# Optimization experiments

Measured on AMD Instinct MI355X. Metric: run time of the kernel, lower is better.

Reference implementation:

```python
import math
import jax, jax.numpy as jnp
import numpy as np

CNT_HEAD, D_IN, D_OUT, D_KEY, D_VALUE = 16, 1024, 1024, 64, 64
BATCH, SEQ = 4, 2048
IS_SCALED, IS_CAUSAL = True, True


def _xavier(key, shape, d1, d2):
    a = math.sqrt(6.0 / (d1 + d2))
    return jax.random.uniform(key, shape, jnp.float32, -a, a)


def setup_inputs() -> dict:
    key = jax.random.key(0)
    kx, kq, kk, kv, ko = jax.random.split(key, 5)
    x = jax.random.normal(kx, (BATCH, SEQ, D_IN), jnp.float32)
    mask = jnp.zeros((BATCH, SEQ), dtype=bool)  # padding mask, True = masked out
    W_q = _xavier(kq, (CNT_HEAD, D_IN, D_KEY), D_IN, CNT_HEAD * D_KEY)
    W_k = _xavier(kk, (CNT_HEAD, D_IN, D_KEY), D_IN, CNT_HEAD * D_KEY)
    W_v = _xavier(kv, (CNT_HEAD, D_IN, D_VALUE), D_IN, CNT_HEAD * D_VALUE)
    W_o = _xavier(ko, (CNT_HEAD, D_VALUE, D_OUT), CNT_HEAD * D_VALUE, D_OUT)
    return {"x": x, "mask": mask, "W_q": W_q, "W_k": W_k, "W_v": W_v, "W_o": W_o}


def reference(x, mask, W_q, W_k, W_v, W_o):
    seq_len = x.shape[-2]
    # per-head projections: (h, d_in, d) x (b, s, d_in) -> (b, h, s, d)
    Q = jnp.einsum('hjk,bsj->bhsk', W_q, x)
    K = jnp.einsum('hjk,bsj->bhsk', W_k, x)
    V = jnp.einsum('hjk,bsj->bhsk', W_v, x)
    # combined mask -> (b, 1, s, s), True = masked
    causal = jnp.triu(jnp.ones((seq_len, seq_len), dtype=bool), k=1)
    if IS_CAUSAL:
        m = mask[..., None, :] | causal  # (b, s, s)
    else:
        m = jnp.broadcast_to(mask[..., None, :], (mask.shape[0], seq_len, seq_len))
    m = m[..., None, :, :]  # (b, 1, s, s)
    scores = jnp.einsum('bhik,bhjk->bhij', Q, K)
    scores = jnp.where(m, -jnp.inf, scores)
    if IS_SCALED:
        scores = scores / math.sqrt(D_KEY)
    weights = jax.nn.softmax(scores, axis=-1)
    values = jnp.einsum('bhij,bhjd->bhid', weights, V)
    return jnp.einsum('hjk,bhlj->blk', W_o, values)
```

## Files before the change

kernel.cpp:

```cpp
#include <hip/hip_runtime.h>
#include <hip/hip_bf16.h>

typedef __attribute__((ext_vector_type(4))) float f32x4;
typedef __attribute__((ext_vector_type(8))) short s16x8;
typedef __attribute__((ext_vector_type(8))) unsigned short u16x8;
typedef __attribute__((ext_vector_type(4))) unsigned short u16x4;

#define BATCH 4
#define SEQ   2048
#define DIN   1024
#define NHEAD 16
#define HD3   3072
#define DOUT  1024

__device__ __forceinline__ unsigned short f2bf(float f) {
  __hip_bfloat16 h = __float2bfloat16(f);
  return __builtin_bit_cast(unsigned short, h);
}

#if __has_builtin(__builtin_amdgcn_exp2f)
__device__ __forceinline__ float fast_exp2(float x) { return __builtin_amdgcn_exp2f(x); }
#else
__device__ __forceinline__ float fast_exp2(float x) { return exp2f(x); }
#endif

typedef const __attribute__((address_space(1))) unsigned int* gas_t;
typedef __attribute__((address_space(3))) unsigned int* las_t;
__device__ __forceinline__ void gload16(const void* g, void* l) {
  __builtin_amdgcn_global_load_lds((gas_t)g, (las_t)l, 16, 0, 0);
}

__device__ __forceinline__ int swz128(int row, int bc) {
  return row * 128 + (((bc & ~15) ^ ((row & 7) << 4)) | (bc & 15));
}

__global__ __launch_bounds__(256) void k_cvt_x(const float* __restrict__ x,
                                               unsigned short* __restrict__ xb, int n4) {
  int i = blockIdx.x * 256 + threadIdx.x;
  int stride = gridDim.x * 256;
  for (; i < n4; i += stride) {
    float4 v = reinterpret_cast<const float4*>(x)[i];
    ushort4 o;
    o.x = f2bf(v.x); o.y = f2bf(v.y); o.z = f2bf(v.z); o.w = f2bf(v.w);
    reinterpret_cast<ushort4*>(xb)[i] = o;
  }
}

__global__ __launch_bounds__(256) void k_cvt_w(const float* __restrict__ W,
                                               unsigned short* __restrict__ dst) {
  __shared__ float t[64][65];
  int h = blockIdx.x, j0 = blockIdx.y * 64;
  int c = threadIdx.x & 63, r0 = threadIdx.x >> 6;
#pragma unroll
  for (int r = r0; r < 64; r += 4)
    t[r][c] = W[h * 65536 + (j0 + r) * 64 + c];
  __syncthreads();
#pragma unroll
  for (int k = r0; k < 64; k += 4)
    dst[(size_t)(h * 64 + k) * 1024 + j0 + c] = f2bf(t[c][k]);
}

__global__ __launch_bounds__(256) void k_cvt_wo(const float* __restrict__ W,
                                                unsigned short* __restrict__ dst) {
  __shared__ float t[64][65];
  int h = blockIdx.x, n0 = blockIdx.y * 64;
  int c = threadIdx.x & 63, r0 = threadIdx.x >> 6;
#pragma unroll
  for (int d = r0; d < 64; d += 4)
    t[d][c] = W[h * 65536 + d * 1024 + n0 + c];
  __syncthreads();
#pragma unroll
  for (int n = r0; n < 64; n += 4)
    dst[(size_t)(n0 + n) * 1024 + h * 64 + c] = f2bf(t[c][n]);
}

__global__ __launch_bounds__(256) void k_transpose_v(const unsigned short* __restrict__ QKV,
                                                     unsigned short* __restrict__ Vt) {
  __shared__ unsigned short t[64 * 80];
  int tid = threadIdx.x;
  int s0 = blockIdx.x * 64;
  int h = blockIdx.y, b = blockIdx.z;
  const unsigned short* src = QKV + (size_t)b * SEQ * HD3 + 2048 + (size_t)h * 64;
#pragma unroll
  for (int c = 0; c < 2; ++c) {
    int slot = tid + c * 256;
    int s = slot >> 3, g = slot & 7;
    u16x8 v = *reinterpret_cast<const u16x8*>(src + (size_t)(s0 + s) * HD3 + g * 8);
    *reinterpret_cast<u16x8*>(&t[s * 80 + (g ^ (s >> 3)) * 8]) = v;
  }
  __syncthreads();
  unsigned short* dst = Vt + (size_t)(b * NHEAD + h) * 64 * SEQ + s0;
#pragma unroll
  for (int c = 0; c < 2; ++c) {
    int slot = tid + c * 256;
    int d = slot >> 3, c8 = slot & 7;
    u16x8 v;
#pragma unroll
    for (int j = 0; j < 8; ++j) {
      int s = c8 * 8 + j;
      v[j] = t[s * 80 + (((d >> 3) ^ c8) * 8) + (d & 7)];
    }
    *reinterpret_cast<u16x8*>(dst + (size_t)d * SEQ + c8 * 8) = v;
  }
}

__device__ __forceinline__ void stout(float* p, float v) { *p = v; }
__device__ __forceinline__ void stout(unsigned short* p, float v) { *p = f2bf(v); }

template <typename OutT>
__global__ __launch_bounds__(256) void gemm_bt(const unsigned short* __restrict__ A,
                                               const unsigned short* __restrict__ Bt,
                                               OutT* __restrict__ C, int M, int N, int K) {
  __shared__ unsigned short As[3][128 * 32];
  __shared__ unsigned short Bs[3][128 * 32];
  int tid = threadIdx.x, w = tid >> 6, lane = tid & 63;
  int lr = lane & 15, lk = lane >> 4;
  int m0 = blockIdx.x * 128, n0 = blockIdx.y * 128;
  int wm = (w >> 1) * 64, wn = (w & 1) * 64;
  const f32x4 z = {0.f, 0.f, 0.f, 0.f};
  f32x4 acc[4][4];
#pragma unroll
  for (int m = 0; m < 4; ++m)
#pragma unroll
    for (int n = 0; n < 4; ++n) acc[m][n] = z;

  int r0 = w * 32 + (lane >> 2);
  int r1 = r0 + 16;
  int scol = (((lane & 3) ^ ((lane >> 2) & 3)) * 8);
  const unsigned short* pA0 = A + (size_t)(m0 + r0) * K + scol;
  const unsigned short* pA1 = A + (size_t)(m0 + r1) * K + scol;
  const unsigned short* pB0 = Bt + (size_t)(n0 + r0) * K + scol;
  const unsigned short* pB1 = Bt + (size_t)(n0 + r1) * K + scol;

#define GSTAGE(bi_, ko_)                                              \
  {                                                                   \
    gload16(pA0 + (ko_), (char*)As[bi_] + (w * 2 + 0) * 1024);        \
    gload16(pB0 + (ko_), (char*)Bs[bi_] + (w * 2 + 0) * 1024);        \
    gload16(pA1 + (ko_), (char*)As[bi_] + (w * 2 + 1) * 1024);        \
    gload16(pB1 + (ko_), (char*)Bs[bi_] + (w * 2 + 1) * 1024);        \
  }

  GSTAGE(0, 0)
  GSTAGE(1, 32)
  asm volatile("s_waitcnt vmcnt(4)" ::: "memory");
  __builtin_amdgcn_s_barrier();
  asm volatile("" ::: "memory");

  const int T = K >> 5;
  int bi = 0;
  int cka = lk ^ (lr & 3);
  for (int t = 0; t < T; ++t) {
    if (t + 2 < T) {
      int bs = bi + 2; if (bs >= 3) bs -= 3;
      GSTAGE(bs, (t + 2) * 32)
    }
    s16x8 af[4], bfr[4];
#pragma unroll
    for (int m = 0; m < 4; ++m)
      af[m] = *reinterpret_cast<const s16x8*>(&As[bi][(wm + m * 16 + lr) * 32 + cka * 8]);
#pragma unroll
    for (int n = 0; n < 4; ++n)
      bfr[n] = *reinterpret_cast<const s16x8*>(&Bs[bi][(wn + n * 16 + lr) * 32 + cka * 8]);
#pragma unroll
    for (int m = 0; m < 4; ++m)
#pragma unroll
      for (int n = 0; n < 4; ++n)
        acc[m][n] = __builtin_amdgcn_mfma_f32_16x16x32_bf16(af[m], bfr[n], acc[m][n], 0, 0, 0);
    asm volatile("s_waitcnt lgkmcnt(0)" ::: "memory");
    if (t + 2 < T)
      asm volatile("s_waitcnt vmcnt(4)" ::: "memory");
    else
      asm volatile("s_waitcnt vmcnt(0)" ::: "memory");
    __builtin_amdgcn_s_barrier();
    asm volatile("" ::: "memory");
    if (++bi >= 3) bi = 0;
  }
#undef GSTAGE

#pragma unroll
  for (int m = 0; m < 4; ++m)
#pragma unroll
    for (int n = 0; n < 4; ++n)
#pragma unroll
      for (int r = 0; r < 4; ++r) {
        int row = m0 + wm + m * 16 + lk * 4 + r;
        int col = n0 + wn + n * 16 + lr;
        stout(&C[(size_t)row * N + col], acc[m][n][r]);
      }
}

__global__ __launch_bounds__(256) void attn_kernel(const unsigned short* __restrict__ QKV,
                                                   const unsigned short* __restrict__ Vt,
                                                   unsigned short* __restrict__ Oa) {
  __shared__ unsigned short Ks[3][64 * 64];
  __shared__ unsigned short Vs[3][64 * 64];
  int tid = threadIdx.x, w = tid >> 6, lane = tid & 63;
  int lr = lane & 15, lk = lane >> 4;
  int bx = blockIdx.x;
  int bh = bx & 63;
  int qbi = 15 - (bx >> 6);
  int h = bh & 15, b = bh >> 4;
  int q0 = qbi * 128 + w * 32;
  const unsigned short* base = QKV + (size_t)b * SEQ * HD3;
  const unsigned short* vtb = Vt + (size_t)(b * NHEAD + h) * 64 * SEQ;
  const float cl = 0.1803368801111204f;
  const f32x4 z = {0.f, 0.f, 0.f, 0.f};

  s16x8 qf[2][2];
#pragma unroll
  for (int mf = 0; mf < 2; ++mf)
#pragma unroll
    for (int kfi = 0; kfi < 2; ++kfi)
      qf[mf][kfi] = *reinterpret_cast<const s16x8*>(
          base + (size_t)(q0 + mf * 16 + lr) * HD3 + h * 64 + kfi * 32 + lk * 8);

  f32x4 o[4][2], lacc[2];
#pragma unroll
  for (int nfd = 0; nfd < 4; ++nfd)
#pragma unroll
    for (int mf = 0; mf < 2; ++mf) o[nfd][mf] = z;
  lacc[0] = z; lacc[1] = z;
  float m_[2] = {-1e30f, -1e30f};
  s16x8 ones;
#pragma unroll
  for (int e = 0; e < 8; ++e) ones[e] = (short)0x3F80;

  const int nt = qbi * 2 + 2;
  int srow0 = w * 16 + (lane >> 3);
  int cb = ((lane & 7) * 16);
  const unsigned short* kSrc = base + 1024 + h * 64;

#define STAGE(kt_, bi_)                                                                   \
  {                                                                                       \
    int kb_ = (kt_) * 64;                                                                 \
    _Pragma("unroll") for (int c = 0; c < 2; ++c) {                                       \
      int rr = srow0 + c * 8;                                                             \
      int cbs = cb ^ ((rr & 7) << 4);                                                     \
      gload16((const char*)(kSrc + (size_t)(kb_ + rr) * HD3) + cbs,                       \
              (char*)&Ks[bi_][0] + (w * 2 + c) * 1024);                                   \
      gload16((const char*)(vtb + (size_t)rr * SEQ + kb_) + cbs,                          \
              (char*)&Vs[bi_][0] + (w * 2 + c) * 1024);                                   \
    }                                                                                     \
  }

  STAGE(0, 0)
  STAGE(1, 1)
  asm volatile("s_waitcnt vmcnt(4)" ::: "memory");
  __builtin_amdgcn_s_barrier();
  asm volatile("" ::: "memory");

  int bi = 0;
  for (int kt = 0; kt < nt; ++kt) {
    if (kt + 2 < nt) {
      int bs = bi + 2; if (bs >= 3) bs -= 3;
      STAGE(kt + 2, bs)
    }
    const char* KB = (const char*)&Ks[bi][0];
    const char* VB = (const char*)&Vs[bi][0];

    s16x8 kfr[4][2];
#pragma unroll
    for (int nf = 0; nf < 4; ++nf)
#pragma unroll
      for (int kfi = 0; kfi < 2; ++kfi)
        kfr[nf][kfi] =
            *reinterpret_cast<const s16x8*>(KB + swz128(nf * 16 + lr, kfi * 64 + lk * 16));

    f32x4 st[4][2];
#pragma unroll
    for (int nf = 0; nf < 4; ++nf)
#pragma unroll
      for (int mf = 0; mf < 2; ++mf)
        st[nf][mf] = __builtin_amdgcn_mfma_f32_16x16x32_bf16(kfr[nf][0], qf[mf][0], z, 0, 0, 0);
#pragma unroll
    for (int nf = 0; nf < 4; ++nf)
#pragma unroll
      for (int mf = 0; mf < 2; ++mf)
        st[nf][mf] =
            __builtin_amdgcn_mfma_f32_16x16x32_bf16(kfr[nf][1], qf[mf][1], st[nf][mf], 0, 0, 0);

    if (kt >= nt - 2) {
      int kb = kt * 64;
#pragma unroll
      for (int nf = 0; nf < 4; ++nf)
#pragma unroll
        for (int mf = 0; mf < 2; ++mf)
#pragma unroll
          for (int r = 0; r < 4; ++r)
            if (kb + nf * 16 + lk * 4 + r > q0 + mf * 16 + lr) st[nf][mf][r] = -1e30f;
    }

    s16x8 pf[2][2];
#pragma unroll
    for (int mf = 0; mf < 2; ++mf) {
      float pm = fmaxf(fmaxf(fmaxf(st[0][mf][0], st[0][mf][1]), fmaxf(st[0][mf][2], st[0][mf][3])),
                       fmaxf(fmaxf(st[1][mf][0], st[1][mf][1]), fmaxf(st[1][mf][2], st[1][mf][3])));
      pm = fmaxf(pm, fmaxf(fmaxf(fmaxf(st[2][mf][0], st[2][mf][1]), fmaxf(st[2][mf][2], st[2][mf][3])),
                           fmaxf(fmaxf(st[3][mf][0], st[3][mf][1]), fmaxf(st[3][mf][2], st[3][mf][3]))));
      pm = fmaxf(pm, __shfl_xor(pm, 16));
      pm = fmaxf(pm, __shfl_xor(pm, 32));
      pm *= cl;
      if (!__all(pm <= m_[mf] + 8.0f)) {
        float mnew = fmaxf(m_[mf], pm);
        float sc = fast_exp2(m_[mf] - mnew);
        m_[mf] = mnew;
#pragma unroll
        for (int nfd = 0; nfd < 4; ++nfd)
#pragma unroll
          for (int r = 0; r < 4; ++r) o[nfd][mf][r] *= sc;
#pragma unroll
        for (int r = 0; r < 4; ++r) lacc[mf][r] *= sc;
      }
      float p[4][4];
#pragma unroll
      for (int nf = 0; nf < 4; ++nf)
#pragma unroll
        for (int r = 0; r < 4; ++r)
          p[nf][r] = fast_exp2(fmaf(st[nf][mf][r], cl, -m_[mf]));
      union { s16x8 v; unsigned short e[8]; } pu0, pu1;
#pragma unroll
      for (int j = 0; j < 4; ++j) {
        pu0.e[j] = f2bf(p[0][j]);
        pu0.e[4 + j] = f2bf(p[1][j]);
        pu1.e[j] = f2bf(p[2][j]);
        pu1.e[4 + j] = f2bf(p[3][j]);
      }
      pf[mf][0] = pu0.v;
      pf[mf][1] = pu1.v;
    }
#pragma unroll
    for (int mf = 0; mf < 2; ++mf)
#pragma unroll
      for (int ks = 0; ks < 2; ++ks)
        lacc[mf] = __builtin_amdgcn_mfma_f32_16x16x32_bf16(ones, pf[mf][ks], lacc[mf], 0, 0, 0);
#pragma unroll
    for (int nfd = 0; nfd < 4; ++nfd)
#pragma unroll
      for (int ks = 0; ks < 2; ++ks) {
        union { s16x8 v; u16x4 half[2]; } vu;
        vu.half[0] =
            *reinterpret_cast<const u16x4*>(VB + swz128(nfd * 16 + lr, ks * 64 + lk * 8));
        vu.half[1] =
            *reinterpret_cast<const u16x4*>(VB + swz128(nfd * 16 + lr, ks * 64 + 32 + lk * 8));
#pragma unroll
        for (int mf = 0; mf < 2; ++mf)
          o[nfd][mf] = __builtin_amdgcn_mfma_f32_16x16x32_bf16(vu.v, pf[mf][ks],
                                                               o[nfd][mf], 0, 0, 0);
      }
    asm volatile("s_waitcnt lgkmcnt(0)" ::: "memory");
    if (kt + 2 < nt)
      asm volatile("s_waitcnt vmcnt(4)" ::: "memory");
    else
      asm volatile("s_waitcnt vmcnt(0)" ::: "memory");
    __builtin_amdgcn_s_barrier();
    asm volatile("" ::: "memory");
    if (++bi >= 3) bi = 0;
  }
#undef STAGE

#pragma unroll
  for (int mf = 0; mf < 2; ++mf) {
    float inv = 1.0f / lacc[mf][0];
    size_t rowoff = (size_t)(b * SEQ + q0 + mf * 16 + lr) * 1024 + h * 64;
#pragma unroll
    for (int nfd = 0; nfd < 4; ++nfd) {
      u16x4 ov;
#pragma unroll
      for (int r = 0; r < 4; ++r) ov[r] = f2bf(o[nfd][mf][r] * inv);
      *reinterpret_cast<u16x4*>(Oa + rowoff + nfd * 16 + lk * 4) = ov;
    }
  }
}

extern "C" void kernel_launch(void* const* d_in, const int* in_sizes, int n_in,
                              void* d_out, int out_size, void* d_ws, size_t ws_size,
                              hipStream_t stream) {
  const float* x  = (const float*)d_in[0];
  const float* Wq = (const float*)d_in[2];
  const float* Wk = (const float*)d_in[3];
  const float* Wv = (const float*)d_in[4];
  const float* Wo = (const float*)d_in[5];
  float* out = (float*)d_out;

  char* ws = (char*)d_ws;
  unsigned short* xb   = (unsigned short*)(ws);
  unsigned short* Wqkv = (unsigned short*)(ws + 16777216);
  unsigned short* Wot  = (unsigned short*)(ws + 23068672);
  unsigned short* QKV  = (unsigned short*)(ws + 25165824);
  unsigned short* Oa   = (unsigned short*)(ws + 75497472);
  unsigned short* Vtp  = xb;

  k_cvt_x<<<2048, 256, 0, stream>>>(x, xb, (BATCH * SEQ * DIN) / 4);
  dim3 wg(16, 16);
  k_cvt_w<<<wg, 256, 0, stream>>>(Wq, Wqkv);
  k_cvt_w<<<wg, 256, 0, stream>>>(Wk, Wqkv + 1024 * 1024);
  k_cvt_w<<<wg, 256, 0, stream>>>(Wv, Wqkv + 2 * 1024 * 1024);
  k_cvt_wo<<<wg, 256, 0, stream>>>(Wo, Wot);

  gemm_bt<unsigned short><<<dim3(64, 24), 256, 0, stream>>>(xb, Wqkv, QKV, 8192, 3072, 1024);
  k_transpose_v<<<dim3(32, NHEAD, BATCH), 256, 0, stream>>>(QKV, Vtp);
  attn_kernel<<<dim3(1024), 256, 0, stream>>>(QKV, Vtp, Oa);
  gemm_bt<float><<<dim3(64, 8), 256, 0, stream>>>(Oa, Wot, out, 8192, 1024, 1024);
}
```

Before: 201.6 us.

## Compute V transposed directly via batched GEMM, skip masked tiles per wave

The V projection is split out of the fused QKV GEMM. It is computed as a batched GEMM (Wv^T times x per batch) that writes V already transposed, so the separate transpose kernel and its round trip through memory go away. In the attention loop, each wave now skips K tiles lying entirely above its causal diagonal and masks only the tiles that straddle it. The MFMA sections are bracketed with s_setprio, and the row-max reduction uses fmax3. This adds a kernel launch, and waves inside a block now do uneven work.

```diff
diff --git a/kernel.cpp b/kernel.cpp
--- a/kernel.cpp
+++ b/kernel.cpp
@@ -10,12 +10,16 @@
 #define SEQ   2048
 #define DIN   1024
 #define NHEAD 16
-#define HD3   3072
+#define QKW   2048
 #define DOUT  1024
 
 __device__ __forceinline__ unsigned short f2bf(float f) {
   __hip_bfloat16 h = __float2bfloat16(f);
   return __builtin_bit_cast(unsigned short, h);
+}
+
+__device__ __forceinline__ float fmax3(float a, float b, float c) {
+  return fmaxf(fmaxf(a, b), c);
 }
 
 #if __has_builtin(__builtin_amdgcn_exp2f)
@@ -74,43 +78,17 @@
     dst[(size_t)(n0 + n) * 1024 + h * 64 + c] = f2bf(t[c][n]);
 }
 
-__global__ __launch_bounds__(256) void k_transpose_v(const unsigned short* __restrict__ QKV,
-                                                     unsigned short* __restrict__ Vt) {
-  __shared__ unsigned short t[64 * 80];
-  int tid = threadIdx.x;
-  int s0 = blockIdx.x * 64;
-  int h = blockIdx.y, b = blockIdx.z;
-  const unsigned short* src = QKV + (size_t)b * SEQ * HD3 + 2048 + (size_t)h * 64;
-#pragma unroll
-  for (int c = 0; c < 2; ++c) {
-    int slot = tid + c * 256;
-    int s = slot >> 3, g = slot & 7;
-    u16x8 v = *reinterpret_cast<const u16x8*>(src + (size_t)(s0 + s) * HD3 + g * 8);
-    *reinterpret_cast<u16x8*>(&t[s * 80 + (g ^ (s >> 3)) * 8]) = v;
-  }
-  __syncthreads();
-  unsigned short* dst = Vt + (size_t)(b * NHEAD + h) * 64 * SEQ + s0;
-#pragma unroll
-  for (int c = 0; c < 2; ++c) {
-    int slot = tid + c * 256;
-    int d = slot >> 3, c8 = slot & 7;
-    u16x8 v;
-#pragma unroll
-    for (int j = 0; j < 8; ++j) {
-      int s = c8 * 8 + j;
-      v[j] = t[s * 80 + (((d >> 3) ^ c8) * 8) + (d & 7)];
-    }
-    *reinterpret_cast<u16x8*>(dst + (size_t)d * SEQ + c8 * 8) = v;
-  }
-}
-
 __device__ __forceinline__ void stout(float* p, float v) { *p = v; }
 __device__ __forceinline__ void stout(unsigned short* p, float v) { *p = f2bf(v); }
 
 template <typename OutT>
 __global__ __launch_bounds__(256) void gemm_bt(const unsigned short* __restrict__ A,
                                                const unsigned short* __restrict__ Bt,
-                                               OutT* __restrict__ C, int M, int N, int K) {
+                                               OutT* __restrict__ C, int M, int N, int K,
+                                               size_t sA, size_t sB, size_t sC) {
+  A += (size_t)blockIdx.z * sA;
+  Bt += (size_t)blockIdx.z * sB;
+  C += (size_t)blockIdx.z * sC;
   __shared__ unsigned short As[3][128 * 32];
   __shared__ unsigned short Bs[3][128 * 32];
   int tid = threadIdx.x, w = tid >> 6, lane = tid & 63;
@@ -189,7 +167,7 @@
       }
 }
 
-__global__ __launch_bounds__(256) void attn_kernel(const unsigned short* __restrict__ QKV,
+__global__ __launch_bounds__(256) void attn_kernel(const unsigned short* __restrict__ QK,
                                                    const unsigned short* __restrict__ Vt,
                                                    unsigned short* __restrict__ Oa) {
   __shared__ unsigned short Ks[3][64 * 64];
@@ -201,7 +179,7 @@
   int qbi = 15 - (bx >> 6);
   int h = bh & 15, b = bh >> 4;
   int q0 = qbi * 128 + w * 32;
-  const unsigned short* base = QKV + (size_t)b * SEQ * HD3;
+  const unsigned short* base = QK + (size_t)b * SEQ * QKW;
   const unsigned short* vtb = Vt + (size_t)(b * NHEAD + h) * 64 * SEQ;
   const float cl = 0.1803368801111204f;
   const f32x4 z = {0.f, 0.f, 0.f, 0.f};
@@ -212,7 +190,7 @@
 #pragma unroll
     for (int kfi = 0; kfi < 2; ++kfi)
       qf[mf][kfi] = *reinterpret_cast<const s16x8*>(
-          base + (size_t)(q0 + mf * 16 + lr) * HD3 + h * 64 + kfi * 32 + lk * 8);
+          base + (size_t)(q0 + mf * 16 + lr) * QKW + h * 64 + kfi * 32 + lk * 8);
 
   f32x4 o[4][2], lacc[2];
 #pragma unroll
@@ -236,7 +214,7 @@
     _Pragma("unroll") for (int c = 0; c < 2; ++c) {                                       \
       int rr = srow0 + c * 8;                                                             \
       int cbs = cb ^ ((rr & 7) << 4);                                                     \
-      gload16((const char*)(kSrc + (size_t)(kb_ + rr) * HD3) + cbs,                       \
+      gload16((const char*)(kSrc + (size_t)(kb_ + rr) * QKW) + cbs,                       \
               (char*)&Ks[bi_][0] + (w * 2 + c) * 1024);                                   \
       gload16((const char*)(vtb + (size_t)rr * SEQ + kb_) + cbs,                          \
               (char*)&Vs[bi_][0] + (w * 2 + c) * 1024);                                   \
@@ -255,98 +233,106 @@
       int bs = bi + 2; if (bs >= 3) bs -= 3;
       STAGE(kt + 2, bs)
     }
-    const char* KB = (const char*)&Ks[bi][0];
-    const char* VB = (const char*)&Vs[bi][0];
-
-    s16x8 kfr[4][2];
-#pragma unroll
-    for (int nf = 0; nf < 4; ++nf)
-#pragma unroll
-      for (int kfi = 0; kfi < 2; ++kfi)
-        kfr[nf][kfi] =
-            *reinterpret_cast<const s16x8*>(KB + swz128(nf * 16 + lr, kfi * 64 + lk * 16));
-
-    f32x4 st[4][2];
-#pragma unroll
-    for (int nf = 0; nf < 4; ++nf)
+    int kb = kt * 64;
+    if (kb <= q0 + 31) {
+      const char* KB = (const char*)&Ks[bi][0];
+      const char* VB = (const char*)&Vs[bi][0];
+
+      s16x8 kfr[4][2];
+#pragma unroll
+      for (int nf = 0; nf < 4; ++nf)
+#pragma unroll
+        for (int kfi = 0; kfi < 2; ++kfi)
+          kfr[nf][kfi] =
+              *reinterpret_cast<const s16x8*>(KB + swz128(nf * 16 + lr, kfi * 64 + lk * 16));
+
+      f32x4 st[4][2];
+      __builtin_amdgcn_s_setprio(1);
+#pragma unroll
+      for (int nf = 0; nf < 4; ++nf)
+#pragma unroll
+        for (int mf = 0; mf < 2; ++mf)
+          st[nf][mf] = __builtin_amdgcn_mfma_f32_16x16x32_bf16(kfr[nf][0], qf[mf][0], z, 0, 0, 0);
+#pragma unroll
+      for (int nf = 0; nf < 4; ++nf)
+#pragma unroll
+        for (int mf = 0; mf < 2; ++mf)
+          st[nf][mf] =
+              __builtin_amdgcn_mfma_f32_16x16x32_bf16(kfr[nf][1], qf[mf][1], st[nf][mf], 0, 0, 0);
+      __builtin_amdgcn_s_setprio(0);
+
+      if (kb + 63 > q0) {
+#pragma unroll
+        for (int nf = 0; nf < 4; ++nf)
+#pragma unroll
+          for (int mf = 0; mf < 2; ++mf)
+#pragma unroll
+            for (int r = 0; r < 4; ++r)
+              if (kb + nf * 16 + lk * 4 + r > q0 + mf * 16 + lr) st[nf][mf][r] = -1e30f;
+      }
+
+      s16x8 pf[2][2];
+#pragma unroll
+      for (int mf = 0; mf < 2; ++mf) {
+        float t0 = fmax3(st[0][mf][0], st[0][mf][1], st[0][mf][2]);
+        float t1 = fmax3(st[0][mf][3], st[1][mf][0], st[1][mf][1]);
+        float t2 = fmax3(st[1][mf][2], st[1][mf][3], st[2][mf][0]);
+        float t3 = fmax3(st[2][mf][1], st[2][mf][2], st[2][mf][3]);
+        float t4 = fmax3(st[3][mf][0], st[3][mf][1], st[3][mf][2]);
+        float pm = fmaxf(fmax3(t0, t1, t2), fmax3(t3, t4, st[3][mf][3]));
+        pm = fmaxf(pm, __shfl_xor(pm, 16));
+        pm = fmaxf(pm, __shfl_xor(pm, 32));
+        pm *= cl;
+        if (!__all(pm <= m_[mf] + 8.0f)) {
+          float mnew = fmaxf(m_[mf], pm);
+          float sc = fast_exp2(m_[mf] - mnew);
+          m_[mf] = mnew;
+#pragma unroll
+          for (int nfd = 0; nfd < 4; ++nfd)
+#pragma unroll
+            for (int r = 0; r < 4; ++r) o[nfd][mf][r] *= sc;
+#pragma unroll
+          for (int r = 0; r < 4; ++r) lacc[mf][r] *= sc;
+        }
+        float p[4][4];
+#pragma unroll
+        for (int nf = 0; nf < 4; ++nf)
+#pragma unroll
+          for (int r = 0; r < 4; ++r)
+            p[nf][r] = fast_exp2(fmaf(st[nf][mf][r], cl, -m_[mf]));
+        union { s16x8 v; unsigned short e[8]; } pu0, pu1;
+#pragma unroll
+        for (int j = 0; j < 4; ++j) {
+          pu0.e[j] = f2bf(p[0][j]);
+          pu0.e[4 + j] = f2bf(p[1][j]);
+          pu1.e[j] = f2bf(p[2][j]);
+          pu1.e[4 + j] = f2bf(p[3][j]);
+        }
+        pf[mf][0] = pu0.v;
+        pf[mf][1] = pu1.v;
+      }
+      __builtin_amdgcn_s_setprio(1);
 #pragma unroll
       for (int mf = 0; mf < 2; ++mf)
-        st[nf][mf] = __builtin_amdgcn_mfma_f32_16x16x32_bf16(kfr[nf][0], qf[mf][0], z, 0, 0, 0);
-#pragma unroll
-    for (int nf = 0; nf < 4; ++nf)
-#pragma unroll
-      for (int mf = 0; mf < 2; ++mf)
-        st[nf][mf] =
-            __builtin_amdgcn_mfma_f32_16x16x32_bf16(kfr[nf][1], qf[mf][1], st[nf][mf], 0, 0, 0);
-
-    if (kt >= nt - 2) {
-      int kb = kt * 64;
-#pragma unroll
-      for (int nf = 0; nf < 4; ++nf)
-#pragma unroll
-        for (int mf = 0; mf < 2; ++mf)
-#pragma unroll
-          for (int r = 0; r < 4; ++r)
-            if (kb + nf * 16 + lk * 4 + r > q0 + mf * 16 + lr) st[nf][mf][r] = -1e30f;
+#pragma unroll
+        for (int ks = 0; ks < 2; ++ks)
+          lacc[mf] = __builtin_amdgcn_mfma_f32_16x16x32_bf16(ones, pf[mf][ks], lacc[mf], 0, 0, 0);
+#pragma unroll
+      for (int nfd = 0; nfd < 4; ++nfd)
+#pragma unroll
+        for (int ks = 0; ks < 2; ++ks) {
+          union { s16x8 v; u16x4 half[2]; } vu;
+          vu.half[0] =
+              *reinterpret_cast<const u16x4*>(VB + swz128(nfd * 16 + lr, ks * 64 + lk * 8));
+          vu.half[1] =
+              *reinterpret_cast<const u16x4*>(VB + swz128(nfd * 16 + lr, ks * 64 + 32 + lk * 8));
+#pragma unroll
+          for (int mf = 0; mf < 2; ++mf)
+            o[nfd][mf] = __builtin_amdgcn_mfma_f32_16x16x32_bf16(vu.v, pf[mf][ks],
+                                                                 o[nfd][mf], 0, 0, 0);
+        }
+      __builtin_amdgcn_s_setprio(0);
     }
-
-    s16x8 pf[2][2];
-#pragma unroll
-    for (int mf = 0; mf < 2; ++mf) {
-      float pm = fmaxf(fmaxf(fmaxf(st[0][mf][0], st[0][mf][1]), fmaxf(st[0][mf][2], st[0][mf][3])),
-                       fmaxf(fmaxf(st[1][mf][0], st[1][mf][1]), fmaxf(st[1][mf][2], st[1][mf][3])));
-      pm = fmaxf(pm, fmaxf(fmaxf(fmaxf(st[2][mf][0], st[2][mf][1]), fmaxf(st[2][mf][2], st[2][mf][3])),
-                           fmaxf(fmaxf(st[3][mf][0], st[3][mf][1]), fmaxf(st[3][mf][2], st[3][mf][3]))));
-      pm = fmaxf(pm, __shfl_xor(pm, 16));
-      pm = fmaxf(pm, __shfl_xor(pm, 32));
-      pm *= cl;
-      if (!__all(pm <= m_[mf] + 8.0f)) {
-        float mnew = fmaxf(m_[mf], pm);
-        float sc = fast_exp2(m_[mf] - mnew);
-        m_[mf] = mnew;
-#pragma unroll
-        for (int nfd = 0; nfd < 4; ++nfd)
-#pragma unroll
-          for (int r = 0; r < 4; ++r) o[nfd][mf][r] *= sc;
-#pragma unroll
-        for (int r = 0; r < 4; ++r) lacc[mf][r] *= sc;
-      }
-      float p[4][4];
-#pragma unroll
-      for (int nf = 0; nf < 4; ++nf)
-#pragma unroll
-        for (int r = 0; r < 4; ++r)
-          p[nf][r] = fast_exp2(fmaf(st[nf][mf][r], cl, -m_[mf]));
-      union { s16x8 v; unsigned short e[8]; } pu0, pu1;
-#pragma unroll
-      for (int j = 0; j < 4; ++j) {
-        pu0.e[j] = f2bf(p[0][j]);
-        pu0.e[4 + j] = f2bf(p[1][j]);
-        pu1.e[j] = f2bf(p[2][j]);
-        pu1.e[4 + j] = f2bf(p[3][j]);
-      }
-      pf[mf][0] = pu0.v;
-      pf[mf][1] = pu1.v;
-    }
-#pragma unroll
-    for (int mf = 0; mf < 2; ++mf)
-#pragma unroll
-      for (int ks = 0; ks < 2; ++ks)
-        lacc[mf] = __builtin_amdgcn_mfma_f32_16x16x32_bf16(ones, pf[mf][ks], lacc[mf], 0, 0, 0);
-#pragma unroll
-    for (int nfd = 0; nfd < 4; ++nfd)
-#pragma unroll
-      for (int ks = 0; ks < 2; ++ks) {
-        union { s16x8 v; u16x4 half[2]; } vu;
-        vu.half[0] =
-            *reinterpret_cast<const u16x4*>(VB + swz128(nfd * 16 + lr, ks * 64 + lk * 8));
-        vu.half[1] =
-            *reinterpret_cast<const u16x4*>(VB + swz128(nfd * 16 + lr, ks * 64 + 32 + lk * 8));
-#pragma unroll
-        for (int mf = 0; mf < 2; ++mf)
-          o[nfd][mf] = __builtin_amdgcn_mfma_f32_16x16x32_bf16(vu.v, pf[mf][ks],
-                                                               o[nfd][mf], 0, 0, 0);
-      }
     asm volatile("s_waitcnt lgkmcnt(0)" ::: "memory");
     if (kt + 2 < nt)
       asm volatile("s_waitcnt vmcnt(4)" ::: "memory");
@@ -383,22 +369,25 @@
   float* out = (float*)d_out;
 
   char* ws = (char*)d_ws;
-  unsigned short* xb   = (unsigned short*)(ws);
-  unsigned short* Wqkv = (unsigned short*)(ws + 16777216);
-  unsigned short* Wot  = (unsigned short*)(ws + 23068672);
-  unsigned short* QKV  = (unsigned short*)(ws + 25165824);
-  unsigned short* Oa   = (unsigned short*)(ws + 75497472);
-  unsigned short* Vtp  = xb;
+  unsigned short* xb  = (unsigned short*)(ws);
+  unsigned short* Wqk = (unsigned short*)(ws + 16777216);
+  unsigned short* Wvt = (unsigned short*)(ws + 20971520);
+  unsigned short* Wot = (unsigned short*)(ws + 23068672);
+  unsigned short* QK  = (unsigned short*)(ws + 25165824);
+  unsigned short* Vt  = (unsigned short*)(ws + 58720256);
+  unsigned short* Oa  = (unsigned short*)(ws + 75497472);
 
   k_cvt_x<<<2048, 256, 0, stream>>>(x, xb, (BATCH * SEQ * DIN) / 4);
   dim3 wg(16, 16);
-  k_cvt_w<<<wg, 256, 0, stream>>>(Wq, Wqkv);
-  k_cvt_w<<<wg, 256, 0, stream>>>(Wk, Wqkv + 1024 * 1024);
-  k_cvt_w<<<wg, 256, 0, stream>>>(Wv, Wqkv + 2 * 1024 * 1024);
+  k_cvt_w<<<wg, 256, 0, stream>>>(Wq, Wqk);
+  k_cvt_w<<<wg, 256, 0, stream>>>(Wk, Wqk + 1024 * 1024);
+  k_cvt_w<<<wg, 256, 0, stream>>>(Wv, Wvt);
   k_cvt_wo<<<wg, 256, 0, stream>>>(Wo, Wot);
 
-  gemm_bt<unsigned short><<<dim3(64, 24), 256, 0, stream>>>(xb, Wqkv, QKV, 8192, 3072, 1024);
-  k_transpose_v<<<dim3(32, NHEAD, BATCH), 256, 0, stream>>>(QKV, Vtp);
-  attn_kernel<<<dim3(1024), 256, 0, stream>>>(QKV, Vtp, Oa);
-  gemm_bt<float><<<dim3(64, 8), 256, 0, stream>>>(Oa, Wot, out, 8192, 1024, 1024);
-}
+  gemm_bt<unsigned short><<<dim3(64, 16), 256, 0, stream>>>(xb, Wqk, QK, 8192, 2048, 1024,
+                                                            0, 0, 0);
+  gemm_bt<unsigned short><<<dim3(8, 16, BATCH), 256, 0, stream>>>(
+      Wvt, xb, Vt, 1024, 2048, 1024, 0, (size_t)SEQ * DIN, (size_t)1024 * SEQ);
+  attn_kernel<<<dim3(1024), 256, 0, stream>>>(QK, Vt, Oa);
+  gemm_bt<float><<<dim3(64, 8), 256, 0, stream>>>(Oa, Wot, out, 8192, 1024, 1024, 0, 0, 0);
+}
```

After: 213.2 us. 5.8% more time.

## Unroll attention loop by 3 buffers, precompute LDS offsets, permute V transpose layout

Applied to the files above, without the earlier changes.

Unrolls the K/V tile loop three times so buffer indices become compile-time constants, and precomputes the swizzled LDS offsets and global-load pointers once per block. It changes the V-transpose layout so each V fragment is read with one 16-byte LDS load instead of two 8-byte loads. It also skips fully masked causal tiles and uses three-input max reductions. The aim is to cut address arithmetic and LDS instruction count in the hot loop, at the cost of larger code and more register pressure.

```diff
diff --git a/kernel.cpp b/kernel.cpp
--- a/kernel.cpp
+++ b/kernel.cpp
@@ -18,6 +18,10 @@
   return __builtin_bit_cast(unsigned short, h);
 }
 
+__device__ __forceinline__ float fmax3(float a, float b, float c) {
+  return fmaxf(fmaxf(a, b), c);
+}
+
 #if __has_builtin(__builtin_amdgcn_exp2f)
 __device__ __forceinline__ float fast_exp2(float x) { return __builtin_amdgcn_exp2f(x); }
 #else
@@ -28,10 +32,6 @@
 typedef __attribute__((address_space(3))) unsigned int* las_t;
 __device__ __forceinline__ void gload16(const void* g, void* l) {
   __builtin_amdgcn_global_load_lds((gas_t)g, (las_t)l, 16, 0, 0);
-}
-
-__device__ __forceinline__ int swz128(int row, int bc) {
-  return row * 128 + (((bc & ~15) ^ ((row & 7) << 4)) | (bc & 15));
 }
 
 __global__ __launch_bounds__(256) void k_cvt_x(const float* __restrict__ x,
@@ -97,8 +97,8 @@
     u16x8 v;
 #pragma unroll
     for (int j = 0; j < 8; ++j) {
-      int s = c8 * 8 + j;
-      v[j] = t[s * 80 + (((d >> 3) ^ c8) * 8) + (d & 7)];
+      int s = ((c8 >> 2) << 5) + ((j >> 2) << 4) + ((c8 & 3) << 2) + (j & 3);
+      v[j] = t[s * 80 + (((d >> 3) ^ (s >> 3)) * 8) + (d & 7)];
     }
     *reinterpret_cast<u16x8*>(dst + (size_t)d * SEQ + c8 * 8) = v;
   }
@@ -226,136 +226,130 @@
   for (int e = 0; e < 8; ++e) ones[e] = (short)0x3F80;
 
   const int nt = qbi * 2 + 2;
+
+  int xr = (lr & 7) << 4;
+  int off8[4][2];
+#pragma unroll
+  for (int nf = 0; nf < 4; ++nf)
+#pragma unroll
+    for (int kfi = 0; kfi < 2; ++kfi)
+      off8[nf][kfi] = (nf * 16 + lr) * 128 + ((kfi * 64 + lk * 16) ^ xr);
+
   int srow0 = w * 16 + (lane >> 3);
-  int cb = ((lane & 7) * 16);
-  const unsigned short* kSrc = base + 1024 + h * 64;
-
-#define STAGE(kt_, bi_)                                                                   \
-  {                                                                                       \
-    int kb_ = (kt_) * 64;                                                                 \
-    _Pragma("unroll") for (int c = 0; c < 2; ++c) {                                       \
-      int rr = srow0 + c * 8;                                                             \
-      int cbs = cb ^ ((rr & 7) << 4);                                                     \
-      gload16((const char*)(kSrc + (size_t)(kb_ + rr) * HD3) + cbs,                       \
-              (char*)&Ks[bi_][0] + (w * 2 + c) * 1024);                                   \
-      gload16((const char*)(vtb + (size_t)rr * SEQ + kb_) + cbs,                          \
-              (char*)&Vs[bi_][0] + (w * 2 + c) * 1024);                                   \
-    }                                                                                     \
-  }
-
-  STAGE(0, 0)
-  STAGE(1, 1)
+  int cbs = ((lane & 7) * 16) ^ ((srow0 & 7) << 4);
+  const char* pk0 = (const char*)(base + 1024 + h * 64 + (size_t)srow0 * HD3) + cbs;
+  const char* pk1 = pk0 + (size_t)8 * HD3 * 2;
+  const char* pv0 = (const char*)(vtb + (size_t)srow0 * SEQ) + cbs;
+  const char* pv1 = pv0 + (size_t)8 * SEQ * 2;
+  const size_t KADV = (size_t)64 * HD3 * 2;
+  const size_t VADV = 128;
+
+#define STAGE(BS)                                                     \
+  {                                                                   \
+    gload16(pk0, (char*)&Ks[(BS)][0] + (w * 2 + 0) * 1024);           \
+    gload16(pv0, (char*)&Vs[(BS)][0] + (w * 2 + 0) * 1024);           \
+    gload16(pk1, (char*)&Ks[(BS)][0] + (w * 2 + 1) * 1024);           \
+    gload16(pv1, (char*)&Vs[(BS)][0] + (w * 2 + 1) * 1024);           \
+    pk0 += KADV; pk1 += KADV; pv0 += VADV; pv1 += VADV;               \
+  }
+
+  STAGE(0)
+  STAGE(1)
   asm volatile("s_waitcnt vmcnt(4)" ::: "memory");
   __builtin_amdgcn_s_barrier();
   asm volatile("" ::: "memory");
 
-  int bi = 0;
-  for (int kt = 0; kt < nt; ++kt) {
-    if (kt + 2 < nt) {
-      int bs = bi + 2; if (bs >= 3) bs -= 3;
-      STAGE(kt + 2, bs)
-    }
-    const char* KB = (const char*)&Ks[bi][0];
-    const char* VB = (const char*)&Vs[bi][0];
-
-    s16x8 kfr[4][2];
-#pragma unroll
-    for (int nf = 0; nf < 4; ++nf)
-#pragma unroll
-      for (int kfi = 0; kfi < 2; ++kfi)
-        kfr[nf][kfi] =
-            *reinterpret_cast<const s16x8*>(KB + swz128(nf * 16 + lr, kfi * 64 + lk * 16));
-
-    f32x4 st[4][2];
-#pragma unroll
-    for (int nf = 0; nf < 4; ++nf)
-#pragma unroll
-      for (int mf = 0; mf < 2; ++mf)
-        st[nf][mf] = __builtin_amdgcn_mfma_f32_16x16x32_bf16(kfr[nf][0], qf[mf][0], z, 0, 0, 0);
-#pragma unroll
-    for (int nf = 0; nf < 4; ++nf)
-#pragma unroll
-      for (int mf = 0; mf < 2; ++mf)
-        st[nf][mf] =
-            __builtin_amdgcn_mfma_f32_16x16x32_bf16(kfr[nf][1], qf[mf][1], st[nf][mf], 0, 0, 0);
-
-    if (kt >= nt - 2) {
-      int kb = kt * 64;
-#pragma unroll
-      for (int nf = 0; nf < 4; ++nf)
-#pragma unroll
-        for (int mf = 0; mf < 2; ++mf)
-#pragma unroll
-          for (int r = 0; r < 4; ++r)
-            if (kb + nf * 16 + lk * 4 + r > q0 + mf * 16 + lr) st[nf][mf][r] = -1e30f;
-    }
-
-    s16x8 pf[2][2];
-#pragma unroll
-    for (int mf = 0; mf < 2; ++mf) {
-      float pm = fmaxf(fmaxf(fmaxf(st[0][mf][0], st[0][mf][1]), fmaxf(st[0][mf][2], st[0][mf][3])),
-                       fmaxf(fmaxf(st[1][mf][0], st[1][mf][1]), fmaxf(st[1][mf][2], st[1][mf][3])));
-      pm = fmaxf(pm, fmaxf(fmaxf(fmaxf(st[2][mf][0], st[2][mf][1]), fmaxf(st[2][mf][2], st[2][mf][3])),
-                           fmaxf(fmaxf(st[3][mf][0], st[3][mf][1]), fmaxf(st[3][mf][2], st[3][mf][3]))));
-      pm = fmaxf(pm, __shfl_xor(pm, 16));
-      pm = fmaxf(pm, __shfl_xor(pm, 32));
-      pm *= cl;
-      if (!__all(pm <= m_[mf] + 8.0f)) {
-        float mnew = fmaxf(m_[mf], pm);
-        float sc = fast_exp2(m_[mf] - mnew);
-        m_[mf] = mnew;
-#pragma unroll
-        for (int nfd = 0; nfd < 4; ++nfd)
-#pragma unroll
-          for (int r = 0; r < 4; ++r) o[nfd][mf][r] *= sc;
-#pragma unroll
-        for (int r = 0; r < 4; ++r) lacc[mf][r] *= sc;
-      }
-      float p[4][4];
-#pragma unroll
-      for (int nf = 0; nf < 4; ++nf)
-#pragma unroll
-        for (int r = 0; r < 4; ++r)
-          p[nf][r] = fast_exp2(fmaf(st[nf][mf][r], cl, -m_[mf]));
-      union { s16x8 v; unsigned short e[8]; } pu0, pu1;
-#pragma unroll
-      for (int j = 0; j < 4; ++j) {
-        pu0.e[j] = f2bf(p[0][j]);
-        pu0.e[4 + j] = f2bf(p[1][j]);
-        pu1.e[j] = f2bf(p[2][j]);
-        pu1.e[4 + j] = f2bf(p[3][j]);
-      }
-      pf[mf][0] = pu0.v;
-      pf[mf][1] = pu1.v;
-    }
-#pragma unroll
-    for (int mf = 0; mf < 2; ++mf)
-#pragma unroll
-      for (int ks = 0; ks < 2; ++ks)
-        lacc[mf] = __builtin_amdgcn_mfma_f32_16x16x32_bf16(ones, pf[mf][ks], lacc[mf], 0, 0, 0);
-#pragma unroll
-    for (int nfd = 0; nfd < 4; ++nfd)
-#pragma unroll
-      for (int ks = 0; ks < 2; ++ks) {
-        union { s16x8 v; u16x4 half[2]; } vu;
-        vu.half[0] =
-            *reinterpret_cast<const u16x4*>(VB + swz128(nfd * 16 + lr, ks * 64 + lk * 8));
-        vu.half[1] =
-            *reinterpret_cast<const u16x4*>(VB + swz128(nfd * 16 + lr, ks * 64 + 32 + lk * 8));
-#pragma unroll
-        for (int mf = 0; mf < 2; ++mf)
-          o[nfd][mf] = __builtin_amdgcn_mfma_f32_16x16x32_bf16(vu.v, pf[mf][ks],
-                                                               o[nfd][mf], 0, 0, 0);
-      }
-    asm volatile("s_waitcnt lgkmcnt(0)" ::: "memory");
-    if (kt + 2 < nt)
-      asm volatile("s_waitcnt vmcnt(4)" ::: "memory");
-    else
-      asm volatile("s_waitcnt vmcnt(0)" ::: "memory");
-    __builtin_amdgcn_s_barrier();
-    asm volatile("" ::: "memory");
-    if (++bi >= 3) bi = 0;
-  }
+#define TILE(BI)                                                                          \
+  {                                                                                       \
+    bool stg = (kt + 2 < nt);                                                             \
+    if (stg) STAGE(((BI) + 2) % 3)                                                        \
+    int kb = kt * 64;                                                                     \
+    if (kb <= q0 + 31) {                                                                  \
+      s16x8 kfr[4][2];                                                                    \
+      _Pragma("unroll") for (int nf = 0; nf < 4; ++nf)                                    \
+      _Pragma("unroll") for (int kfi = 0; kfi < 2; ++kfi)                                 \
+        kfr[nf][kfi] = *reinterpret_cast<const s16x8*>(                                   \
+            (const char*)&Ks[(BI)][0] + off8[nf][kfi]);                                   \
+      f32x4 st[4][2];                                                                     \
+      _Pragma("unroll") for (int nf = 0; nf < 4; ++nf)                                    \
+      _Pragma("unroll") for (int mf = 0; mf < 2; ++mf)                                    \
+        st[nf][mf] = __builtin_amdgcn_mfma_f32_16x16x32_bf16(kfr[nf][0], qf[mf][0], z, 0, 0, 0); \
+      _Pragma("unroll") for (int nf = 0; nf < 4; ++nf)                                    \
+      _Pragma("unroll") for (int mf = 0; mf < 2; ++mf)                                    \
+        st[nf][mf] = __builtin_amdgcn_mfma_f32_16x16x32_bf16(kfr[nf][1], qf[mf][1],       \
+                                                             st[nf][mf], 0, 0, 0);        \
+      if (kb + 63 > q0) {                                                                 \
+        _Pragma("unroll") for (int nf = 0; nf < 4; ++nf)                                  \
+        _Pragma("unroll") for (int mf = 0; mf < 2; ++mf)                                  \
+        _Pragma("unroll") for (int r = 0; r < 4; ++r)                                     \
+          if (kb + nf * 16 + lk * 4 + r > q0 + mf * 16 + lr) st[nf][mf][r] = -1e30f;      \
+      }                                                                                   \
+      s16x8 pf[2][2];                                                                     \
+      _Pragma("unroll") for (int mf = 0; mf < 2; ++mf) {                                  \
+        float t0 = fmax3(st[0][mf][0], st[0][mf][1], st[0][mf][2]);                       \
+        float t1 = fmax3(st[0][mf][3], st[1][mf][0], st[1][mf][1]);                       \
+        float t2 = fmax3(st[1][mf][2], st[1][mf][3], st[2][mf][0]);                       \
+        float t3 = fmax3(st[2][mf][1], st[2][mf][2], st[2][mf][3]);                       \
+        float t4 = fmax3(st[3][mf][0], st[3][mf][1], st[3][mf][2]);                       \
+        float pm = fmaxf(fmax3(t0, t1, t2), fmax3(t3, t4, st[3][mf][3]));                 \
+        pm = fmaxf(pm, __shfl_xor(pm, 16));                                               \
+        pm = fmaxf(pm, __shfl_xor(pm, 32));                                               \
+        pm *= cl;                                                                         \
+        if (!__all(pm <= m_[mf] + 8.0f)) {                                                \
+          float mnew = fmaxf(m_[mf], pm);                                                 \
+          float sc = fast_exp2(m_[mf] - mnew);                                            \
+          m_[mf] = mnew;                                                                  \
+          _Pragma("unroll") for (int nfd = 0; nfd < 4; ++nfd)                             \
+          _Pragma("unroll") for (int r = 0; r < 4; ++r) o[nfd][mf][r] *= sc;              \
+          _Pragma("unroll") for (int r = 0; r < 4; ++r) lacc[mf][r] *= sc;                \
+        }                                                                                 \
+        float p[4][4];                                                                    \
+        _Pragma("unroll") for (int nf = 0; nf < 4; ++nf)                                  \
+        _Pragma("unroll") for (int r = 0; r < 4; ++r)                                     \
+          p[nf][r] = fast_exp2(fmaf(st[nf][mf][r], cl, -m_[mf]));                         \
+        union { s16x8 v; unsigned short e[8]; } pu0, pu1;                                 \
+        _Pragma("unroll") for (int j = 0; j < 4; ++j) {                                   \
+          pu0.e[j] = f2bf(p[0][j]);                                                       \
+          pu0.e[4 + j] = f2bf(p[1][j]);                                                   \
+          pu1.e[j] = f2bf(p[2][j]);                                                       \
+          pu1.e[4 + j] = f2bf(p[3][j]);                                                   \
+        }                                                                                 \
+        pf[mf][0] = pu0.v;                                                                \
+        pf[mf][1] = pu1.v;                                                                \
+      }                                                                                   \
+      _Pragma("unroll") for (int mf = 0; mf < 2; ++mf)                                    \
+      _Pragma("unroll") for (int ks = 0; ks < 2; ++ks)                                    \
+        lacc[mf] = __builtin_amdgcn_mfma_f32_16x16x32_bf16(ones, pf[mf][ks],              \
+                                                           lacc[mf], 0, 0, 0);            \
+      _Pragma("unroll") for (int nfd = 0; nfd < 4; ++nfd)                                 \
+      _Pragma("unroll") for (int ks = 0; ks < 2; ++ks) {                                  \
+        s16x8 vf = *reinterpret_cast<const s16x8*>(                                       \
+            (const char*)&Vs[(BI)][0] + off8[nfd][ks]);                                   \
+        _Pragma("unroll") for (int mf = 0; mf < 2; ++mf)                                  \
+          o[nfd][mf] = __builtin_amdgcn_mfma_f32_16x16x32_bf16(vf, pf[mf][ks],            \
+                                                               o[nfd][mf], 0, 0, 0);      \
+      }                                                                                   \
+    }                                                                                     \
+    asm volatile("s_waitcnt lgkmcnt(0)" ::: "memory");                                    \
+    if (stg)                                                                              \
+      asm volatile("s_waitcnt vmcnt(4)" ::: "memory");                                    \
+    else                                                                                  \
+      asm volatile("s_waitcnt vmcnt(0)" ::: "memory");                                    \
+    __builtin_amdgcn_s_barrier();                                                         \
+    asm volatile("" ::: "memory");                                                        \
+    ++kt;                                                                                 \
+  }
+
+  int kt = 0;
+  for (;;) {
+    TILE(0)
+    if (kt == nt) break;
+    TILE(1)
+    if (kt == nt) break;
+    TILE(2)
+    if (kt == nt) break;
+  }
+#undef TILE
 #undef STAGE
 
 #pragma unroll
```

After: 200.7 us. Within noise of the previous version (-0.4%).
